# Kernel optimization log

Measured on AMD Instinct MI355X. Metric: run time of the kernel, lower is better.

The kernel has to match this reference:

```python
import jax, jax.numpy as jnp
import numpy as np

REG_MAX = 16
TOPK = 13
ALPHA = 1.0
BETA = 6.0
MATCH_W = 0.5
IOU_W = 7.5
DFL_W = 1.5
EPS = 1e-7
NEG_INF = -1e30


def _iou(b1, b2):
    # xyxy IoU, broadcastable [..., 4]
    x1 = jnp.maximum(b1[..., 0], b2[..., 0]); y1 = jnp.maximum(b1[..., 1], b2[..., 1])
    x2 = jnp.minimum(b1[..., 2], b2[..., 2]); y2 = jnp.minimum(b1[..., 3], b2[..., 3])
    inter = jnp.maximum(x2 - x1, 0.0) * jnp.maximum(y2 - y1, 0.0)
    a1 = (b1[..., 2] - b1[..., 0]) * (b1[..., 3] - b1[..., 1])
    a2 = (b2[..., 2] - b2[..., 0]) * (b2[..., 3] - b2[..., 1])
    return inter / (a1 + a2 - inter + EPS)


def _ciou(b1, b2):
    iou = _iou(b1, b2)
    w1 = b1[..., 2] - b1[..., 0]; h1 = b1[..., 3] - b1[..., 1]
    w2 = b2[..., 2] - b2[..., 0]; h2 = b2[..., 3] - b2[..., 1]
    cw = jnp.maximum(b1[..., 2], b2[..., 2]) - jnp.minimum(b1[..., 0], b2[..., 0])
    ch = jnp.maximum(b1[..., 3], b2[..., 3]) - jnp.minimum(b1[..., 1], b2[..., 1])
    c2 = cw * cw + ch * ch + EPS
    rho2 = ((b2[..., 0] + b2[..., 2] - b1[..., 0] - b1[..., 2]) ** 2
            + (b2[..., 1] + b2[..., 3] - b1[..., 1] - b1[..., 3]) ** 2) / 4.0
    v = (4.0 / jnp.pi ** 2) * (jnp.arctan(w2 / (h2 + EPS)) - jnp.arctan(w1 / (h1 + EPS))) ** 2
    a = jax.lax.stop_gradient(v / (v - iou + (1.0 + EPS)))
    return iou - (rho2 / c2 + v * a)


def _per_sample(ps, pb, bd, gtb, gtl, vcm, anchor, stride):
    # ps [N,C], pb [N,4], bd [N,4*R], gtb [M,4], gtl [M], vcm [C] bool
    N, C = ps.shape
    M = gtb.shape[0]
    lab = jnp.clip(gtl, 0, C - 1)
    gt_valid = (gtl >= 0) & (gtl < C) & vcm[lab]
    ax, ay = anchor[:, 0], anchor[:, 1]
    inside = ((ax[None, :] >= gtb[:, 0:1]) & (ax[None, :] <= gtb[:, 2:3])
              & (ay[None, :] >= gtb[:, 1:2]) & (ay[None, :] <= gtb[:, 3:4]))  # [M,N]
    iou_mn = _iou(pb[None, :, :], gtb[:, None, :])                             # [M,N]
    cls_mn = jax.nn.sigmoid(ps[:, lab]).T                                      # [M,N]
    align = jnp.where(inside & gt_valid[:, None], cls_mn ** ALPHA * iou_mn ** BETA, NEG_INF)
    top_vals, top_idx = jax.lax.top_k(align, TOPK)                             # [M,K]
    cand = jnp.full((M, N), NEG_INF, ps.dtype).at[jnp.arange(M)[:, None], top_idx].set(top_vals)
    best = cand.max(0)          # final metric per anchor
    mg = cand.argmax(0)         # winning GT (first max == earliest GT, matching loop order)
    fg = best > -1.0            # align >= 0 always; non-candidates stay at NEG_INF
    m_lab = jnp.clip(gtl[mg], 0, C - 1)
    ov = iou_mn[mg, jnp.arange(N)]
    fgf = fg.astype(ps.dtype)
    tgt_scores = jax.nn.one_hot(m_lab, C, dtype=ps.dtype) * (jnp.maximum(ov, 0.1) * fgf)[:, None]
    tb = jnp.where(fg[:, None], gtb[mg], pb)   # safe target boxes (masked out when not fg)

    # classification BCE over valid classes (mean)
    bce = jnp.maximum(ps, 0.0) - ps * tgt_scores + jnp.log1p(jnp.exp(-jnp.abs(ps)))
    vc = vcm.astype(ps.dtype)
    match = (bce * vc[None, :]).sum() / (N * jnp.maximum(vc.sum(), 1.0))

    cnt = fg.sum()
    ciou_v = _ciou(pb, tb)
    iou_loss = jnp.where(cnt > 0, ((1.0 - ciou_v) * fgf).sum() / jnp.maximum(cnt, 1), 0.0)
    miou_sum = (_iou(pb, tb) * fgf).sum()
    probs = jax.nn.sigmoid(ps)
    pos_sum = (probs[jnp.arange(N), m_lab] * fgf).sum()

    # DFL
    d = jnp.concatenate([anchor - tb[:, :2], tb[:, 2:] - anchor], -1) / stride  # [N,4]
    d = jnp.clip(d, 0.0, REG_MAX - 1 - 0.01)
    tl = d.astype(jnp.int32)
    tr = jnp.minimum(tl + 1, REG_MAX - 1)
    wl = tr.astype(ps.dtype) - d
    wr = 1.0 - wl
    logp = jax.nn.log_softmax(bd.reshape(N, 4, REG_MAX), -1)
    ll = -jnp.take_along_axis(logp, tl[..., None], -1)[..., 0]
    lr = -jnp.take_along_axis(logp, tr[..., None], -1)[..., 0]
    dfl = jnp.where(cnt > 0, ((ll * wl + lr * wr) * fgf[:, None]).sum() / jnp.maximum(cnt * 4, 1), 0.0)

    mx = jnp.where(vcm[None, :], probs, NEG_INF).max(-1)
    neg_sum = (mx * (1.0 - fgf)).sum()
    neg_cnt = N - cnt
    return match, iou_loss, dfl, cnt, neg_cnt, pos_sum, neg_sum, miou_sum


def setup_inputs() -> dict:
    key = jax.random.key(0)
    B, N, C, M, R = 16, 8400, 80, 64, REG_MAX
    ks = jax.random.split(key, 7)
    pts, sts = [], []
    for s in (8, 16, 32):
        n = 640 // s
        g = (np.arange(n) + 0.5) * s
        xv, yv = np.meshgrid(g, g)
        pts.append(np.stack([xv.ravel(), yv.ravel()], 1))
        sts.append(np.full((n * n, 1), s, np.float32))
    anchor_points = jnp.asarray(np.concatenate(pts).astype(np.float32))  # [8400,2]
    stride_tensor = jnp.asarray(np.concatenate(sts))                      # [8400,1]
    c = anchor_points[None] + jax.random.normal(ks[0], (B, N, 2)) * stride_tensor[None]
    wh = jax.random.uniform(ks[1], (B, N, 2), minval=8.0, maxval=128.0)
    pred_boxes = jnp.concatenate([jnp.clip(c - wh / 2, 0.0, 640.0),
                                  jnp.clip(c + wh / 2, 0.0, 640.0)], -1)
    gc = jax.random.uniform(ks[2], (B, M, 2), minval=64.0, maxval=576.0)
    gwh = jax.random.uniform(ks[3], (B, M, 2), minval=16.0, maxval=128.0)
    gt_boxes = jnp.concatenate([gc - gwh / 2, gc + gwh / 2], -1)
    gt_labels = jax.random.randint(ks[4], (B, M), 0, C)
    class_mask = jnp.ones((B, C), bool)
    pred_scores = jax.random.normal(ks[5], (B, N, C))
    box_distribution = jax.random.normal(ks[6], (B, N, 4 * R))
    return {"pred_scores": pred_scores, "pred_boxes": pred_boxes,
            "anchor_points": anchor_points, "stride_tensor": stride_tensor,
            "box_distribution": box_distribution, "gt_boxes": gt_boxes,
            "gt_labels": gt_labels, "class_mask": class_mask}


def reference(pred_scores, pred_boxes, anchor_points, stride_tensor,
              box_distribution, gt_boxes, gt_labels, class_mask):
    B = pred_scores.shape[0]
    f = lambda ps, pb, bd, gtb, gtl, vcm: _per_sample(ps, pb, bd, gtb, gtl, vcm,
                                                      anchor_points, stride_tensor)
    match, iou_l, dfl, cnt, ncnt, psum, nsum, misum = jax.vmap(f)(
        pred_scores, pred_boxes, box_distribution, gt_boxes, gt_labels, class_mask)
    tot_pos = cnt.sum()
    tot_neg = ncnt.sum()
    total_match = match.sum(); total_iou = iou_l.sum(); total_dfl = dfl.sum()
    loss = (MATCH_W * total_match + IOU_W * total_iou + DFL_W * total_dfl) / B
    mean_pos = psum.sum() / jnp.maximum(tot_pos, 1)
    mean_neg = nsum.sum() / jnp.maximum(tot_neg, 1)
    mean_miou = misum.sum() / jnp.maximum(tot_pos, 1)
    return (loss, total_match / B, total_iou / B, total_dfl / B,
            tot_pos.astype(jnp.float32), mean_pos, mean_neg, mean_miou)
```

## Files before the change

### kernel.cpp

```cpp
#include <hip/hip_runtime.h>
#include <stdint.h>

#define TOPK 13
#define NEG_INF_F (-1e30f)
#define EPSF 1e-7f
#define L2EF 1.4426950408889634f
#define LN2F 0.6931471805599453f
#define MAXCAND 2048
#define MAXB_LDS 64

__device__ __forceinline__ int mask_at(const uint8_t* __restrict__ raw, int i) {
    bool as_u8 = (raw[1] | raw[2] | raw[3]) != 0;
    return as_u8 ? (raw[i] != 0) : (((const int*)raw)[i] != 0);
}

__device__ __forceinline__ float iou_pair(float ax1, float ay1, float ax2, float ay2,
                                          float bx1, float by1, float bx2, float by2) {
    float x1 = fmaxf(ax1, bx1), y1 = fmaxf(ay1, by1);
    float x2 = fminf(ax2, bx2), y2 = fminf(ay2, by2);
    float inter = fmaxf(x2 - x1, 0.f) * fmaxf(y2 - y1, 0.f);
    float a1 = (ax2 - ax1) * (ay2 - ay1);
    float a2 = (bx2 - bx1) * (by2 - by1);
    return inter / (a1 + a2 - inter + EPSF);
}

__device__ __forceinline__ float sigmoid_fast(float s) {
    return 1.f / (1.f + exp2f(-s * L2EF));
}
__device__ __forceinline__ float softplus_bce(float s) {
    float t = exp2f(-fabsf(s) * L2EF);
    return fmaxf(s, 0.f) + log2f(1.f + t) * LN2F;
}

__device__ __forceinline__ void assign_wave(
    const float* __restrict__ ps, const float* __restrict__ pb,
    const float* __restrict__ gtb, const int* __restrict__ gtl,
    const uint8_t* __restrict__ mraw,
    unsigned long long* __restrict__ best, unsigned* __restrict__ list,
    int B, int N, int C, int M, int t, int lane) {
    int b = t % B;
    int m = t / B;

    int lbl = gtl[b * M + m];
    int lab = min(max(lbl, 0), C - 1);
    if (!((lbl >= 0) && (lbl < C) && (mask_at(mraw, b * C + lab) != 0))) return;

    float4 g = ((const float4*)gtb)[(size_t)b * M + m];

    const int   n0_[3]  = { 0, 6400, 8000 };
    const int   dim_[3] = { 80, 40, 20 };
    const float sv_[3]  = { 8.f, 16.f, 32.f };

    int ix0[3], iy0[3], ww[3], pre[4];
    pre[0] = 0;
#pragma unroll
    for (int l = 0; l < 3; ++l) {
        float s = sv_[l]; int d = dim_[l];
        int ax0 = max(0,     (int)ceilf (g.x / s - 0.5f));
        int ax1 = min(d - 1, (int)floorf(g.z / s - 0.5f));
        int ay0 = max(0,     (int)ceilf (g.y / s - 0.5f));
        int ay1 = min(d - 1, (int)floorf(g.w / s - 0.5f));
        int w = max(0, ax1 - ax0 + 1);
        int h = max(0, ay1 - ay0 + 1);
        ix0[l] = ax0; iy0[l] = ay0; ww[l] = w;
        pre[l + 1] = pre[l] + w * h;
    }
    int tot = pre[3];
    if (tot == 0) return;

    const float* psb = ps + (size_t)b * N * C + lab;
    const float4* pbb = (const float4*)pb + (size_t)b * N;

    float lv[TOPK];
    int   li[TOPK];
#pragma unroll
    for (int j = 0; j < TOPK; ++j) { lv[j] = NEG_INF_F; li[j] = -1; }

    for (int tt = lane; tt < tot; tt += 64) {
        int l = (tt >= pre[1]) + (tt >= pre[2]);
        int r = tt - pre[l];
        int w = ww[l];
        int iy = r / w, ix = r - iy * w;
        int gx = ix0[l] + ix, gy = iy0[l] + iy;
        int n = n0_[l] + gy * dim_[l] + gx;
        float4 p = pbb[n];
        float iou = iou_pair(p.x, p.y, p.z, p.w, g.x, g.y, g.z, g.w);
        float sc = psb[(size_t)n * C];
        float i3 = iou * iou * iou;
        float val = sigmoid_fast(sc) * i3 * i3;
        if (val > lv[TOPK - 1]) {
            bool placed = false;
#pragma unroll
            for (int j = TOPK - 1; j >= 1; --j) {
                if (!placed) {
                    if (val > lv[j - 1]) { lv[j] = lv[j - 1]; li[j] = li[j - 1]; }
                    else { lv[j] = val; li[j] = n; placed = true; }
                }
            }
            if (!placed) { lv[0] = val; li[0] = n; }
        }
    }

    unsigned key = 0xFFFFFFFFu - (unsigned)m;
    unsigned long long* bb = best + (size_t)b * N;
    unsigned* myslots = list + ((size_t)b * M + m) * TOPK;
    int rounds = min(tot, TOPK);
    for (int p = 0; p < rounds; ++p) {
        float bv = lv[0]; int bn = li[0];
        for (int off = 32; off > 0; off >>= 1) {
            float ov = __shfl_down(bv, off, 64);
            int   on = __shfl_down(bn, off, 64);
            if (ov > bv || (ov == bv && (unsigned)on < (unsigned)bn)) { bv = ov; bn = on; }
        }
        bv = __shfl(bv, 0, 64);
        bn = __shfl(bn, 0, 64);
        if (bn < 0) break;
        if (li[0] == bn) {
            unsigned long long pk =
                ((unsigned long long)__float_as_uint(lv[0]) << 32) | (unsigned long long)key;
            atomicMax(bb + bn, pk);
            myslots[p] = (unsigned)bn + 1u;
#pragma unroll
            for (int j = 0; j < TOPK - 1; ++j) { lv[j] = lv[j + 1]; li[j] = li[j + 1]; }
            lv[TOPK - 1] = NEG_INF_F; li[TOPK - 1] = -1;
        }
    }
}

__global__ __launch_bounds__(256, 1) void fused_a_k(
    const float* __restrict__ ps, const float* __restrict__ pb,
    const float* __restrict__ gtb, const int* __restrict__ gtl,
    const uint8_t* __restrict__ mraw,
    unsigned long long* __restrict__ best, unsigned* __restrict__ list,
    float* __restrict__ sigbuf, float* __restrict__ partials,
    int B, int N, int C, int M, int asgb, int nb) {
    if ((int)blockIdx.x < asgb) {
        int t = blockIdx.x * 4 + (threadIdx.x >> 6);
        if (t < B * M)
            assign_wave(ps, pb, gtb, gtl, mraw, best, list,
                        B, N, C, M, t, threadIdx.x & 63);
        return;
    }
    int bi = blockIdx.x - asgb;
    int b = bi / nb;
    int n = (bi % nb) * 256 + threadIdx.x;

    __shared__ int smask[256];
    __shared__ int s_notall;
    __shared__ float sredA[4], sredB[4];
    if (threadIdx.x == 0) s_notall = 0;
    __syncthreads();
    for (int c = threadIdx.x; c < C && c < 256; c += 256) {
        int v = mask_at(mraw, b * C + c);
        smask[c] = v;
        if (!v) s_notall = 1;
    }
    __syncthreads();
    bool allm = (s_notall == 0);

    float acc0 = 0.f, acc3 = 0.f;
    if (n < N) {
        const float* psr = ps + ((size_t)b * N + n) * C;
        float bce_sum = 0.f, smax = NEG_INF_F;

        if (C == 80 && allm) {
            const float4* p4 = (const float4*)psr;
            float4 s4[20];
#pragma unroll
            for (int i = 0; i < 20; ++i) s4[i] = p4[i];
#pragma unroll
            for (int i = 0; i < 20; ++i) {
                bce_sum += softplus_bce(s4[i].x) + softplus_bce(s4[i].y) +
                           softplus_bce(s4[i].z) + softplus_bce(s4[i].w);
                smax = fmaxf(smax, fmaxf(fmaxf(s4[i].x, s4[i].y), fmaxf(s4[i].z, s4[i].w)));
            }
        } else if (allm) {
            int c4 = C & ~3;
            for (int c = 0; c < c4; c += 4) {
                float4 s4 = *(const float4*)(psr + c);
                bce_sum += softplus_bce(s4.x) + softplus_bce(s4.y) +
                           softplus_bce(s4.z) + softplus_bce(s4.w);
                smax = fmaxf(smax, fmaxf(fmaxf(s4.x, s4.y), fmaxf(s4.z, s4.w)));
            }
            for (int c = c4; c < C; ++c) {
                float s = psr[c];
                bce_sum += softplus_bce(s);
                smax = fmaxf(smax, s);
            }
        } else {
            for (int c = 0; c < C; ++c) {
                float s = psr[c];
                if (smask[c]) { bce_sum += softplus_bce(s); smax = fmaxf(smax, s); }
            }
        }
        float sg = sigmoid_fast(smax);
        sigbuf[(size_t)b * N + n] = sg;
        acc0 = bce_sum;
        acc3 = sg;
    }

    int lane = threadIdx.x & 63, wid = threadIdx.x >> 6;
    float v0 = acc0, v3 = acc3;
    for (int off = 32; off > 0; off >>= 1) {
        v0 += __shfl_down(v0, off, 64);
        v3 += __shfl_down(v3, off, 64);
    }
    if (lane == 0) { sredA[wid] = v0; sredB[wid] = v3; }
    __syncthreads();
    if (threadIdx.x == 0) {
        atomicAdd(&partials[b * 8 + 0], sredA[0] + sredA[1] + sredA[2] + sredA[3]);
        atomicAdd(&partials[b * 8 + 3], sredB[0] + sredB[1] + sredB[2] + sredB[3]);
    }
}

__global__ __launch_bounds__(256, 1) void fused_b_k(
    const float* __restrict__ ps, const float* __restrict__ pb,
    const float* __restrict__ anch, const float* __restrict__ strd,
    const float* __restrict__ bd, const float* __restrict__ gtb,
    const int* __restrict__ gtl, const uint8_t* __restrict__ mraw,
    const unsigned long long* __restrict__ best, const float* __restrict__ sigbuf,
    const unsigned* __restrict__ list,
    float* __restrict__ partials, unsigned int* __restrict__ done_ctr,
    float* __restrict__ out, int B, int N, int C, int M) {
    __shared__ float sacc[MAXB_LDS * 8];
    __shared__ int s_last;
    bool use_lds = (B <= MAXB_LDS);
    if (use_lds)
        for (int i = threadIdx.x; i < B * 8; i += 256) sacc[i] = 0.f;
    __syncthreads();

    int idx = blockIdx.x * 256 + threadIdx.x;
    int cap = B * M * TOPK;
    bool active = false;
    int b = 0, n = 0, mg = 0;
    if (idx < cap) {
        unsigned e = list[idx];
        if (e != 0u) {
            n = (int)(e - 1u);
            b = idx / (M * TOPK);
            int m_claim = (idx / TOPK) % M;
            unsigned long long pk = best[(size_t)b * N + n];
            mg = (int)(0xFFFFFFFFu - (unsigned)(pk & 0xFFFFFFFFull));
            active = (mg == m_claim);
        }
    }

    if (active) {
        int lbl = gtl[b * M + mg];
        int m_lab = min(max(lbl, 0), C - 1);

        const float* bdr = bd + ((size_t)b * N + n) * 64;
        const float4* bq4 = (const float4*)bdr;
        float4 bq[16];
#pragma unroll
        for (int i = 0; i < 16; ++i) bq[i] = bq4[i];
        float4 p = ((const float4*)pb)[(size_t)b * N + n];
        float4 g = ((const float4*)gtb)[(size_t)b * M + mg];
        float2 an = ((const float2*)anch)[n];
        float stv = strd[n];
        float slab = ps[((size_t)b * N + n) * C + m_lab];
        float sg = sigbuf[(size_t)b * N + n];

        float ov = iou_pair(p.x, p.y, p.z, p.w, g.x, g.y, g.z, g.w);
        float acc0 = -fmaxf(ov, 0.1f) * slab;
        float acc2 = sigmoid_fast(slab);
        float acc4 = ov;
        float w1 = p.z - p.x, h1 = p.w - p.y;
        float w2 = g.z - g.x, h2 = g.w - g.y;
        float cw = fmaxf(p.z, g.z) - fminf(p.x, g.x);
        float ch = fmaxf(p.w, g.w) - fminf(p.y, g.y);
        float c2 = cw * cw + ch * ch + EPSF;
        float dx = g.x + g.z - p.x - p.z;
        float dy = g.y + g.w - p.y - p.w;
        float rho2 = (dx * dx + dy * dy) * 0.25f;
        const float PI = 3.14159265358979323846f;
        float dv = atanf(w2 / (h2 + EPSF)) - atanf(w1 / (h1 + EPSF));
        float v = (4.f / (PI * PI)) * dv * dv;
        float a = v / (v - ov + 1.f + EPSF);
        float acc5 = 1.f - (ov - (rho2 / c2 + v * a));
        float dall[4] = { (an.x - g.x) / stv, (an.y - g.y) / stv,
                          (g.z - an.x) / stv, (g.w - an.y) / stv };
        float dfl = 0.f;
#pragma unroll
        for (int k = 0; k < 4; ++k) {
            float4 q0 = bq[k * 4 + 0], q1 = bq[k * 4 + 1];
            float4 q2 = bq[k * 4 + 2], q3 = bq[k * 4 + 3];
            float mxv = fmaxf(fmaxf(fmaxf(q0.x, q0.y), fmaxf(q0.z, q0.w)),
                              fmaxf(fmaxf(q1.x, q1.y), fmaxf(q1.z, q1.w)));
            mxv = fmaxf(mxv, fmaxf(fmaxf(fmaxf(q2.x, q2.y), fmaxf(q2.z, q2.w)),
                                    fmaxf(fmaxf(q3.x, q3.y), fmaxf(q3.z, q3.w))));
            float se = exp2f((q0.x - mxv) * L2EF) + exp2f((q0.y - mxv) * L2EF) +
                       exp2f((q0.z - mxv) * L2EF) + exp2f((q0.w - mxv) * L2EF) +
                       exp2f((q1.x - mxv) * L2EF) + exp2f((q1.y - mxv) * L2EF) +
                       exp2f((q1.z - mxv) * L2EF) + exp2f((q1.w - mxv) * L2EF) +
                       exp2f((q2.x - mxv) * L2EF) + exp2f((q2.y - mxv) * L2EF) +
                       exp2f((q2.z - mxv) * L2EF) + exp2f((q2.w - mxv) * L2EF) +
                       exp2f((q3.x - mxv) * L2EF) + exp2f((q3.y - mxv) * L2EF) +
                       exp2f((q3.z - mxv) * L2EF) + exp2f((q3.w - mxv) * L2EF);
            float lse = mxv + log2f(se) * LN2F;
            float d = fminf(fmaxf(dall[k], 0.f), 14.99f);
            int tl = (int)d;
            int tr = min(tl + 1, 15);
            float wl = (float)tr - d;
            float xtl = bdr[k * 16 + tl];
            float xtr = bdr[k * 16 + tr];
            dfl += (lse - xtl) * wl + (lse - xtr) * (1.f - wl);
        }
        float accs[7] = { acc0, 1.f, acc2, -sg, acc4, acc5, dfl };
        if (use_lds) {
#pragma unroll
            for (int j = 0; j < 7; ++j) atomicAdd(&sacc[b * 8 + j], accs[j]);
        } else {
#pragma unroll
            for (int j = 0; j < 7; ++j) atomicAdd(&partials[b * 8 + j], accs[j]);
        }
    }
    __syncthreads();
    if (use_lds)
        for (int i = threadIdx.x; i < B * 8; i += 256)
            if (sacc[i] != 0.f) atomicAdd(&partials[i], sacc[i]);
    __syncthreads();

    if (threadIdx.x == 0) {
        __threadfence();
        unsigned r = atomicAdd(done_ctr, 1u);
        s_last = (r == gridDim.x - 1u) ? 1 : 0;
    }
    __syncthreads();
    if (!s_last) return;
    if (threadIdx.x >= 64) return;
    __threadfence();

    int fl = threadIdx.x;
    float tm = 0, ti = 0, td = 0, tp = 0, tneg = 0, pos = 0, neg = 0, miou = 0;
    for (int s = fl; s < B; s += 64) {
        float vcs = 0.f;
        for (int c = 0; c < C; ++c) vcs += mask_at(mraw, s * C + c) ? 1.f : 0.f;
        const float* pr = partials + s * 8;
        float p0 = __hip_atomic_load(&pr[0], __ATOMIC_RELAXED, __HIP_MEMORY_SCOPE_AGENT);
        float p1 = __hip_atomic_load(&pr[1], __ATOMIC_RELAXED, __HIP_MEMORY_SCOPE_AGENT);
        float p2 = __hip_atomic_load(&pr[2], __ATOMIC_RELAXED, __HIP_MEMORY_SCOPE_AGENT);
        float p3 = __hip_atomic_load(&pr[3], __ATOMIC_RELAXED, __HIP_MEMORY_SCOPE_AGENT);
        float p4 = __hip_atomic_load(&pr[4], __ATOMIC_RELAXED, __HIP_MEMORY_SCOPE_AGENT);
        float p5 = __hip_atomic_load(&pr[5], __ATOMIC_RELAXED, __HIP_MEMORY_SCOPE_AGENT);
        float p6 = __hip_atomic_load(&pr[6], __ATOMIC_RELAXED, __HIP_MEMORY_SCOPE_AGENT);
        float cnt = p1;
        tm += p0 / ((float)N * fmaxf(vcs, 1.f));
        ti += (cnt > 0.f) ? p5 / fmaxf(cnt, 1.f) : 0.f;
        td += (cnt > 0.f) ? p6 / fmaxf(cnt * 4.f, 1.f) : 0.f;
        tp += cnt; tneg += (float)N - cnt;
        pos += p2; neg += p3; miou += p4;
    }
    for (int off = 32; off > 0; off >>= 1) {
        tm += __shfl_down(tm, off, 64);   ti += __shfl_down(ti, off, 64);
        td += __shfl_down(td, off, 64);   tp += __shfl_down(tp, off, 64);
        tneg += __shfl_down(tneg, off, 64); pos += __shfl_down(pos, off, 64);
        neg += __shfl_down(neg, off, 64); miou += __shfl_down(miou, off, 64);
    }
    if (fl == 0) {
        float Bf = (float)B;
        out[0] = (0.5f * tm + 7.5f * ti + 1.5f * td) / Bf;
        out[1] = tm / Bf;
        out[2] = ti / Bf;
        out[3] = td / Bf;
        out[4] = tp;
        out[5] = pos / fmaxf(tp, 1.f);
        out[6] = neg / fmaxf(tneg, 1.f);
        out[7] = miou / fmaxf(tp, 1.f);
    }
}

__global__ __launch_bounds__(256) void assign_topk_k(
    const float* __restrict__ ps, const float* __restrict__ pb,
    const float* __restrict__ anch, const float* __restrict__ gtb,
    const int* __restrict__ gtl, const uint8_t* __restrict__ mraw,
    unsigned long long* __restrict__ best, int B, int N, int C, int M) {
    int b = blockIdx.x % B;
    int m = blockIdx.x / B;

    __shared__ float cval[MAXCAND];
    __shared__ int   cidx[MAXCAND];
    __shared__ int   scnt;
    if (threadIdx.x == 0) scnt = 0;

    int lbl = gtl[b * M + m];
    int lab = min(max(lbl, 0), C - 1);
    bool valid = (lbl >= 0) && (lbl < C) && (mask_at(mraw, b * C + lab) != 0);
    __syncthreads();

    if (valid) {
        float4 g = ((const float4*)gtb)[(size_t)b * M + m];
        const float* psb = ps + (size_t)b * N * C + lab;
        const float4* pbb = (const float4*)pb + (size_t)b * N;
        for (int n = threadIdx.x; n < N; n += 256) {
            float2 a = ((const float2*)anch)[n];
            if (a.x < g.x || a.x > g.z || a.y < g.y || a.y > g.w) continue;
            float4 p = pbb[n];
            float iou = iou_pair(p.x, p.y, p.z, p.w, g.x, g.y, g.z, g.w);
            float s = psb[(size_t)n * C];
            float i3 = iou * iou * iou;
            float val = sigmoid_fast(s) * i3 * i3;
            int slot = atomicAdd(&scnt, 1);
            if (slot < MAXCAND) { cval[slot] = val; cidx[slot] = n; }
        }
    }
    __syncthreads();
    if (!valid || threadIdx.x >= 64) return;

    int total = min(scnt, MAXCAND);
    if (total == 0) return;
    int lane = threadIdx.x;

    float lv[TOPK];
    int   li[TOPK];
#pragma unroll
    for (int j = 0; j < TOPK; ++j) { lv[j] = NEG_INF_F; li[j] = -1; }
    for (int i = lane; i < total; i += 64) {
        float v = cval[i]; int ix = cidx[i];
        if (v > lv[TOPK - 1]) {
            bool placed = false;
#pragma unroll
            for (int j = TOPK - 1; j >= 1; --j) {
                if (!placed) {
                    if (v > lv[j - 1]) { lv[j] = lv[j - 1]; li[j] = li[j - 1]; }
                    else { lv[j] = v; li[j] = ix; placed = true; }
                }
            }
            if (!placed) { lv[0] = v; li[0] = ix; }
        }
    }

    unsigned key = 0xFFFFFFFFu - (unsigned)m;
    unsigned long long* bb = best + (size_t)b * N;
    int rounds = min(total, TOPK);
    for (int p = 0; p < rounds; ++p) {
        float bv = lv[0]; int bn = li[0];
        for (int off = 32; off > 0; off >>= 1) {
            float ov = __shfl_down(bv, off, 64);
            int   on = __shfl_down(bn, off, 64);
            if (ov > bv || (ov == bv && (unsigned)on < (unsigned)bn)) { bv = ov; bn = on; }
        }
        bv = __shfl(bv, 0, 64);
        bn = __shfl(bn, 0, 64);
        if (bn < 0) break;
        if (li[0] == bn) {
            unsigned long long pk =
                ((unsigned long long)__float_as_uint(lv[0]) << 32) | (unsigned long long)key;
            atomicMax(bb + bn, pk);
#pragma unroll
            for (int j = 0; j < TOPK - 1; ++j) { lv[j] = lv[j + 1]; li[j] = li[j + 1]; }
            lv[TOPK - 1] = NEG_INF_F; li[TOPK - 1] = -1;
        }
    }
}

__global__ __launch_bounds__(256, 1) void per_anchor_k(
    const float* __restrict__ ps, const float* __restrict__ pb,
    const float* __restrict__ anch, const float* __restrict__ strd,
    const float* __restrict__ bd, const float* __restrict__ gtb,
    const int* __restrict__ gtl, const uint8_t* __restrict__ mraw,
    const unsigned long long* __restrict__ best,
    float* __restrict__ partials, int B, int N, int C, int M) {
    int b = blockIdx.y;
    int n = blockIdx.x * 256 + threadIdx.x;

    __shared__ int smask[256];
    __shared__ int s_notall;
    __shared__ float sred[4 * 8];
    if (threadIdx.x == 0) s_notall = 0;
    __syncthreads();
    for (int c = threadIdx.x; c < C && c < 256; c += 256) {
        int v = mask_at(mraw, b * C + c);
        smask[c] = v;
        if (!v) s_notall = 1;
    }
    __syncthreads();
    bool allm = (s_notall == 0);

    float acc0 = 0, acc1 = 0, acc2 = 0, acc3 = 0, acc4 = 0, acc5 = 0, acc6 = 0;

    if (n < N) {
        unsigned long long pk = best[(size_t)b * N + n];
        bool fg = (pk != 0ull);
        int mg = fg ? (int)(0xFFFFFFFFu - (unsigned)(pk & 0xFFFFFFFFull)) : 0;
        int lbl = gtl[b * M + mg];
        int m_lab = min(max(lbl, 0), C - 1);

        const float* psr = ps + ((size_t)b * N + n) * C;
        float bce_sum = 0.f, smax = NEG_INF_F;

        if (C == 80 && allm) {
            const float4* p4 = (const float4*)psr;
            float4 s4[20];
#pragma unroll
            for (int i = 0; i < 20; ++i) s4[i] = p4[i];
#pragma unroll
            for (int i = 0; i < 20; ++i) {
                bce_sum += softplus_bce(s4[i].x) + softplus_bce(s4[i].y) +
                           softplus_bce(s4[i].z) + softplus_bce(s4[i].w);
                smax = fmaxf(smax, fmaxf(fmaxf(s4[i].x, s4[i].y), fmaxf(s4[i].z, s4[i].w)));
            }
        } else if (allm) {
            int c4 = C & ~3;
            for (int c = 0; c < c4; c += 4) {
                float4 s4 = *(const float4*)(psr + c);
                bce_sum += softplus_bce(s4.x) + softplus_bce(s4.y) +
                           softplus_bce(s4.z) + softplus_bce(s4.w);
                smax = fmaxf(smax, fmaxf(fmaxf(s4.x, s4.y), fmaxf(s4.z, s4.w)));
            }
            for (int c = c4; c < C; ++c) {
                float s = psr[c];
                bce_sum += softplus_bce(s);
                smax = fmaxf(smax, s);
            }
        } else {
            for (int c = 0; c < C; ++c) {
                float s = psr[c];
                if (smask[c]) { bce_sum += softplus_bce(s); smax = fmaxf(smax, s); }
            }
        }

        acc1 = fg ? 1.f : 0.f;
        acc3 = fg ? 0.f : sigmoid_fast(smax);

        if (fg) {
            const float* bdr = bd + ((size_t)b * N + n) * 64;
            const float4* bq4 = (const float4*)bdr;
            float4 bq[16];
#pragma unroll
            for (int i = 0; i < 16; ++i) bq[i] = bq4[i];
            float4 p = ((const float4*)pb)[(size_t)b * N + n];
            float4 g = ((const float4*)gtb)[(size_t)b * M + mg];
            float2 an = ((const float2*)anch)[n];
            float stv = strd[n];
            float slab = psr[m_lab];

            float ov = iou_pair(p.x, p.y, p.z, p.w, g.x, g.y, g.z, g.w);
            bce_sum -= fmaxf(ov, 0.1f) * slab;
            acc2 = sigmoid_fast(slab);
            acc4 = ov;
            float w1 = p.z - p.x, h1 = p.w - p.y;
            float w2 = g.z - g.x, h2 = g.w - g.y;
            float cw = fmaxf(p.z, g.z) - fminf(p.x, g.x);
            float ch = fmaxf(p.w, g.w) - fminf(p.y, g.y);
            float c2 = cw * cw + ch * ch + EPSF;
            float dx = g.x + g.z - p.x - p.z;
            float dy = g.y + g.w - p.y - p.w;
            float rho2 = (dx * dx + dy * dy) * 0.25f;
            const float PI = 3.14159265358979323846f;
            float dv = atanf(w2 / (h2 + EPSF)) - atanf(w1 / (h1 + EPSF));
            float v = (4.f / (PI * PI)) * dv * dv;
            float a = v / (v - ov + 1.f + EPSF);
            acc5 = 1.f - (ov - (rho2 / c2 + v * a));
            float dall[4] = { (an.x - g.x) / stv, (an.y - g.y) / stv,
                              (g.z - an.x) / stv, (g.w - an.y) / stv };
            float dfl = 0.f;
#pragma unroll
            for (int k = 0; k < 4; ++k) {
                float4 q0 = bq[k * 4 + 0], q1 = bq[k * 4 + 1];
                float4 q2 = bq[k * 4 + 2], q3 = bq[k * 4 + 3];
                float mxv = fmaxf(fmaxf(fmaxf(q0.x, q0.y), fmaxf(q0.z, q0.w)),
                                  fmaxf(fmaxf(q1.x, q1.y), fmaxf(q1.z, q1.w)));
                mxv = fmaxf(mxv, fmaxf(fmaxf(fmaxf(q2.x, q2.y), fmaxf(q2.z, q2.w)),
                                        fmaxf(fmaxf(q3.x, q3.y), fmaxf(q3.z, q3.w))));
                float se = exp2f((q0.x - mxv) * L2EF) + exp2f((q0.y - mxv) * L2EF) +
                           exp2f((q0.z - mxv) * L2EF) + exp2f((q0.w - mxv) * L2EF) +
                           exp2f((q1.x - mxv) * L2EF) + exp2f((q1.y - mxv) * L2EF) +
                           exp2f((q1.z - mxv) * L2EF) + exp2f((q1.w - mxv) * L2EF) +
                           exp2f((q2.x - mxv) * L2EF) + exp2f((q2.y - mxv) * L2EF) +
                           exp2f((q2.z - mxv) * L2EF) + exp2f((q2.w - mxv) * L2EF) +
                           exp2f((q3.x - mxv) * L2EF) + exp2f((q3.y - mxv) * L2EF) +
                           exp2f((q3.z - mxv) * L2EF) + exp2f((q3.w - mxv) * L2EF);
                float lse = mxv + log2f(se) * LN2F;
                float d = fminf(fmaxf(dall[k], 0.f), 14.99f);
                int tl = (int)d;
                int tr = min(tl + 1, 15);
                float wl = (float)tr - d;
                float xtl = bdr[k * 16 + tl];
                float xtr = bdr[k * 16 + tr];
                dfl += (lse - xtl) * wl + (lse - xtr) * (1.f - wl);
            }
            acc6 = dfl;
        }
        acc0 = bce_sum;
    }

    int lane = threadIdx.x & 63, wid = threadIdx.x >> 6;
    float accs[7] = { acc0, acc1, acc2, acc3, acc4, acc5, acc6 };
#pragma unroll
    for (int j = 0; j < 7; ++j) {
        float v = accs[j];
        for (int off = 32; off > 0; off >>= 1) v += __shfl_down(v, off, 64);
        if (lane == 0) sred[wid * 8 + j] = v;
    }
    __syncthreads();
    if (threadIdx.x < 7) {
        float s = sred[0 * 8 + threadIdx.x] + sred[1 * 8 + threadIdx.x] +
                  sred[2 * 8 + threadIdx.x] + sred[3 * 8 + threadIdx.x];
        atomicAdd(&partials[b * 8 + threadIdx.x], s);
    }
}

__global__ void finalize_k(const float* __restrict__ partials, const uint8_t* __restrict__ mraw,
                           float* __restrict__ out, int B, int N, int C) {
    int lane = threadIdx.x;
    float tm = 0, ti = 0, td = 0, tp = 0, tneg = 0, pos = 0, neg = 0, miou = 0;
    if (lane < B) {
        float vcs = 0.f;
        for (int c = 0; c < C; ++c) vcs += mask_at(mraw, lane * C + c) ? 1.f : 0.f;
        const float* pr = partials + lane * 8;
        float cnt = pr[1];
        tm = pr[0] / ((float)N * fmaxf(vcs, 1.f));
        ti = (cnt > 0.f) ? pr[5] / fmaxf(cnt, 1.f) : 0.f;
        td = (cnt > 0.f) ? pr[6] / fmaxf(cnt * 4.f, 1.f) : 0.f;
        tp = cnt; tneg = (float)N - cnt;
        pos = pr[2]; neg = pr[3]; miou = pr[4];
    }
    for (int off = 32; off > 0; off >>= 1) {
        tm += __shfl_down(tm, off, 64);   ti += __shfl_down(ti, off, 64);
        td += __shfl_down(td, off, 64);   tp += __shfl_down(tp, off, 64);
        tneg += __shfl_down(tneg, off, 64); pos += __shfl_down(pos, off, 64);
        neg += __shfl_down(neg, off, 64); miou += __shfl_down(miou, off, 64);
    }
    if (lane == 0) {
        float Bf = (float)B;
        out[0] = (0.5f * tm + 7.5f * ti + 1.5f * td) / Bf;
        out[1] = tm / Bf;
        out[2] = ti / Bf;
        out[3] = td / Bf;
        out[4] = tp;
        out[5] = pos / fmaxf(tp, 1.f);
        out[6] = neg / fmaxf(tneg, 1.f);
        out[7] = miou / fmaxf(tp, 1.f);
    }
}

extern "C" void kernel_launch(void* const* d_in, const int* in_sizes, int n_in,
                              void* d_out, int out_size, void* d_ws, size_t ws_size,
                              hipStream_t stream) {
    const float* ps   = (const float*)d_in[0];
    const float* pb   = (const float*)d_in[1];
    const float* anch = (const float*)d_in[2];
    const float* strd = (const float*)d_in[3];
    const float* bd   = (const float*)d_in[4];
    const float* gtb  = (const float*)d_in[5];
    const int*   gtl  = (const int*)d_in[6];
    const uint8_t* cmsk = (const uint8_t*)d_in[7];

    int N = in_sizes[2] / 2;
    int B = in_sizes[1] / (4 * N);
    int C = in_sizes[0] / (B * N);
    int M = in_sizes[6] / B;

    size_t bestBytes = (size_t)B * N * sizeof(unsigned long long);
    size_t off1 = (bestBytes + 255) & ~(size_t)255;
    size_t partBytes = (size_t)B * 8 * sizeof(float);
    size_t off2 = (off1 + partBytes + 255) & ~(size_t)255;
    size_t off3 = off2 + 256;
    size_t listBytes = (size_t)B * M * TOPK * sizeof(unsigned);
    size_t zeroBytes = (off3 + listBytes + 255) & ~(size_t)255;
    unsigned long long* best = (unsigned long long*)d_ws;
    float* partials = (float*)((char*)d_ws + off1);
    unsigned int* done_ctr = (unsigned int*)((char*)d_ws + off2);
    unsigned int* list = (unsigned int*)((char*)d_ws + off3);
    float* sigbuf = (float*)((char*)d_ws + zeroBytes);

    hipMemsetAsync(d_ws, 0, zeroBytes, stream);

    int nb = (N + 255) / 256;
    if (N == 8400) {
        int asgb = (B * M + 3) / 4;
        fused_a_k<<<asgb + B * nb, 256, 0, stream>>>(ps, pb, gtb, gtl, cmsk,
                                                     best, list, sigbuf,
                                                     partials, B, N, C, M, asgb, nb);
        int cap = B * M * TOPK;
        int nblk = (cap + 255) / 256;
        fused_b_k<<<nblk, 256, 0, stream>>>(ps, pb, anch, strd, bd, gtb, gtl, cmsk,
                                            best, sigbuf, list,
                                            partials, done_ctr, (float*)d_out, B, N, C, M);
    } else {
        assign_topk_k<<<B * M, 256, 0, stream>>>(ps, pb, anch, gtb, gtl, cmsk, best, B, N, C, M);
        dim3 gB(nb, B);
        per_anchor_k<<<gB, 256, 0, stream>>>(ps, pb, anch, strd, bd, gtb, gtl, cmsk, best,
                                             partials, B, N, C, M);
        finalize_k<<<1, 64, 0, stream>>>(partials, cmsk, (float*)d_out, B, N, C);
    }
}
```

Measured before the change: 152.0 us.

## Merge assign/scan and foreground-loss kernels into one launch with grid-wide spin barrier

Fuses the two kernels on the N==8400 path into one mega-kernel. Each block bumps an atomic counter once its assignment or scan phase finishes. Scan blocks whose index falls within the candidate list then spin-wait on that counter before doing the foreground CIoU/DFL work. This removes one kernel launch and the gap between launches, but it relies on every block being co-resident to avoid deadlock. It also adds spin-wait latency and holds back some blocks.

```diff
diff --git a/kernel.cpp b/kernel.cpp
--- a/kernel.cpp
+++ b/kernel.cpp
@@ -127,27 +127,35 @@
     }
 }
 
-__global__ __launch_bounds__(256, 1) void fused_a_k(
+__global__ __launch_bounds__(256, 1) void mega_k(
     const float* __restrict__ ps, const float* __restrict__ pb,
-    const float* __restrict__ gtb, const int* __restrict__ gtl,
-    const uint8_t* __restrict__ mraw,
+    const float* __restrict__ anch, const float* __restrict__ strd,
+    const float* __restrict__ bd, const float* __restrict__ gtb,
+    const int* __restrict__ gtl, const uint8_t* __restrict__ mraw,
     unsigned long long* __restrict__ best, unsigned* __restrict__ list,
     float* __restrict__ sigbuf, float* __restrict__ partials,
-    int B, int N, int C, int M, int asgb, int nb) {
+    unsigned* __restrict__ a_done, unsigned* __restrict__ b_done,
+    float* __restrict__ out,
+    int B, int N, int C, int M, int asgb, int nb, int nscan, int cap) {
+    __shared__ int smask[256];
+    __shared__ int s_notall;
+    __shared__ float sredA[4], sredB[4];
+    __shared__ float sacc[MAXB_LDS * 8];
+    __shared__ int s_flag;
+
     if ((int)blockIdx.x < asgb) {
         int t = blockIdx.x * 4 + (threadIdx.x >> 6);
         if (t < B * M)
             assign_wave(ps, pb, gtb, gtl, mraw, best, list,
                         B, N, C, M, t, threadIdx.x & 63);
+        __syncthreads();
+        if (threadIdx.x == 0) { __threadfence(); atomicAdd(a_done, 1u); }
         return;
     }
     int bi = blockIdx.x - asgb;
     int b = bi / nb;
     int n = (bi % nb) * 256 + threadIdx.x;
 
-    __shared__ int smask[256];
-    __shared__ int s_notall;
-    __shared__ float sredA[4], sredB[4];
     if (threadIdx.x == 0) s_notall = 0;
     __syncthreads();
     for (int c = threadIdx.x; c < C && c < 256; c += 256) {
@@ -200,350 +208,79 @@
     }
 
     int lane = threadIdx.x & 63, wid = threadIdx.x >> 6;
-    float v0 = acc0, v3 = acc3;
-    for (int off = 32; off > 0; off >>= 1) {
-        v0 += __shfl_down(v0, off, 64);
-        v3 += __shfl_down(v3, off, 64);
-    }
-    if (lane == 0) { sredA[wid] = v0; sredB[wid] = v3; }
+    {
+        float v0 = acc0, v3 = acc3;
+        for (int off = 32; off > 0; off >>= 1) {
+            v0 += __shfl_down(v0, off, 64);
+            v3 += __shfl_down(v3, off, 64);
+        }
+        if (lane == 0) { sredA[wid] = v0; sredB[wid] = v3; }
+    }
     __syncthreads();
     if (threadIdx.x == 0) {
         atomicAdd(&partials[b * 8 + 0], sredA[0] + sredA[1] + sredA[2] + sredA[3]);
         atomicAdd(&partials[b * 8 + 3], sredB[0] + sredB[1] + sredB[2] + sredB[3]);
-    }
-}
-
-__global__ __launch_bounds__(256, 1) void fused_b_k(
-    const float* __restrict__ ps, const float* __restrict__ pb,
-    const float* __restrict__ anch, const float* __restrict__ strd,
-    const float* __restrict__ bd, const float* __restrict__ gtb,
-    const int* __restrict__ gtl, const uint8_t* __restrict__ mraw,
-    const unsigned long long* __restrict__ best, const float* __restrict__ sigbuf,
-    const unsigned* __restrict__ list,
-    float* __restrict__ partials, unsigned int* __restrict__ done_ctr,
-    float* __restrict__ out, int B, int N, int C, int M) {
-    __shared__ float sacc[MAXB_LDS * 8];
-    __shared__ int s_last;
+        __threadfence();
+        atomicAdd(a_done, 1u);
+    }
+
+    int base = bi * 256;
     bool use_lds = (B <= MAXB_LDS);
-    if (use_lds)
-        for (int i = threadIdx.x; i < B * 8; i += 256) sacc[i] = 0.f;
-    __syncthreads();
-
-    int idx = blockIdx.x * 256 + threadIdx.x;
-    int cap = B * M * TOPK;
-    bool active = false;
-    int b = 0, n = 0, mg = 0;
-    if (idx < cap) {
-        unsigned e = list[idx];
-        if (e != 0u) {
-            n = (int)(e - 1u);
-            b = idx / (M * TOPK);
-            int m_claim = (idx / TOPK) % M;
-            unsigned long long pk = best[(size_t)b * N + n];
-            mg = (int)(0xFFFFFFFFu - (unsigned)(pk & 0xFFFFFFFFull));
-            active = (mg == m_claim);
-        }
-    }
-
-    if (active) {
-        int lbl = gtl[b * M + mg];
-        int m_lab = min(max(lbl, 0), C - 1);
-
-        const float* bdr = bd + ((size_t)b * N + n) * 64;
-        const float4* bq4 = (const float4*)bdr;
-        float4 bq[16];
-#pragma unroll
-        for (int i = 0; i < 16; ++i) bq[i] = bq4[i];
-        float4 p = ((const float4*)pb)[(size_t)b * N + n];
-        float4 g = ((const float4*)gtb)[(size_t)b * M + mg];
-        float2 an = ((const float2*)anch)[n];
-        float stv = strd[n];
-        float slab = ps[((size_t)b * N + n) * C + m_lab];
-        float sg = sigbuf[(size_t)b * N + n];
-
-        float ov = iou_pair(p.x, p.y, p.z, p.w, g.x, g.y, g.z, g.w);
-        float acc0 = -fmaxf(ov, 0.1f) * slab;
-        float acc2 = sigmoid_fast(slab);
-        float acc4 = ov;
-        float w1 = p.z - p.x, h1 = p.w - p.y;
-        float w2 = g.z - g.x, h2 = g.w - g.y;
-        float cw = fmaxf(p.z, g.z) - fminf(p.x, g.x);
-        float ch = fmaxf(p.w, g.w) - fminf(p.y, g.y);
-        float c2 = cw * cw + ch * ch + EPSF;
-        float dx = g.x + g.z - p.x - p.z;
-        float dy = g.y + g.w - p.y - p.w;
-        float rho2 = (dx * dx + dy * dy) * 0.25f;
-        const float PI = 3.14159265358979323846f;
-        float dv = atanf(w2 / (h2 + EPSF)) - atanf(w1 / (h1 + EPSF));
-        float v = (4.f / (PI * PI)) * dv * dv;
-        float a = v / (v - ov + 1.f + EPSF);
-        float acc5 = 1.f - (ov - (rho2 / c2 + v * a));
-        float dall[4] = { (an.x - g.x) / stv, (an.y - g.y) / stv,
-                          (g.z - an.x) / stv, (g.w - an.y) / stv };
-        float dfl = 0.f;
-#pragma unroll
-        for (int k = 0; k < 4; ++k) {
-            float4 q0 = bq[k * 4 + 0], q1 = bq[k * 4 + 1];
-            float4 q2 = bq[k * 4 + 2], q3 = bq[k * 4 + 3];
-            float mxv = fmaxf(fmaxf(fmaxf(q0.x, q0.y), fmaxf(q0.z, q0.w)),
-                              fmaxf(fmaxf(q1.x, q1.y), fmaxf(q1.z, q1.w)));
-            mxv = fmaxf(mxv, fmaxf(fmaxf(fmaxf(q2.x, q2.y), fmaxf(q2.z, q2.w)),
-                                    fmaxf(fmaxf(q3.x, q3.y), fmaxf(q3.z, q3.w))));
-            float se = exp2f((q0.x - mxv) * L2EF) + exp2f((q0.y - mxv) * L2EF) +
-                       exp2f((q0.z - mxv) * L2EF) + exp2f((q0.w - mxv) * L2EF) +
-                       exp2f((q1.x - mxv) * L2EF) + exp2f((q1.y - mxv) * L2EF) +
-                       exp2f((q1.z - mxv) * L2EF) + exp2f((q1.w - mxv) * L2EF) +
-                       exp2f((q2.x - mxv) * L2EF) + exp2f((q2.y - mxv) * L2EF) +
-                       exp2f((q2.z - mxv) * L2EF) + exp2f((q2.w - mxv) * L2EF) +
-                       exp2f((q3.x - mxv) * L2EF) + exp2f((q3.y - mxv) * L2EF) +
-                       exp2f((q3.z - mxv) * L2EF) + exp2f((q3.w - mxv) * L2EF);
-            float lse = mxv + log2f(se) * LN2F;
-            float d = fminf(fmaxf(dall[k], 0.f), 14.99f);
-            int tl = (int)d;
-            int tr = min(tl + 1, 15);
-            float wl = (float)tr - d;
-            float xtl = bdr[k * 16 + tl];
-            float xtr = bdr[k * 16 + tr];
-            dfl += (lse - xtl) * wl + (lse - xtr) * (1.f - wl);
-        }
-        float accs[7] = { acc0, 1.f, acc2, -sg, acc4, acc5, dfl };
-        if (use_lds) {
-#pragma unroll
-            for (int j = 0; j < 7; ++j) atomicAdd(&sacc[b * 8 + j], accs[j]);
-        } else {
-#pragma unroll
-            for (int j = 0; j < 7; ++j) atomicAdd(&partials[b * 8 + j], accs[j]);
-        }
-    }
-    __syncthreads();
-    if (use_lds)
-        for (int i = threadIdx.x; i < B * 8; i += 256)
-            if (sacc[i] != 0.f) atomicAdd(&partials[i], sacc[i]);
-    __syncthreads();
-
-    if (threadIdx.x == 0) {
+    if (base < cap) {
+        if (threadIdx.x == 0) {
+            int a_target = asgb + nscan;
+            while ((int)__hip_atomic_load(a_done, __ATOMIC_ACQUIRE,
+                                          __HIP_MEMORY_SCOPE_AGENT) < a_target)
+                __builtin_amdgcn_s_sleep(8);
+            s_flag = 1;
+        }
+        __syncthreads();
         __threadfence();
-        unsigned r = atomicAdd(done_ctr, 1u);
-        s_last = (r == gridDim.x - 1u) ? 1 : 0;
-    }
-    __syncthreads();
-    if (!s_last) return;
-    if (threadIdx.x >= 64) return;
-    __threadfence();
-
-    int fl = threadIdx.x;
-    float tm = 0, ti = 0, td = 0, tp = 0, tneg = 0, pos = 0, neg = 0, miou = 0;
-    for (int s = fl; s < B; s += 64) {
-        float vcs = 0.f;
-        for (int c = 0; c < C; ++c) vcs += mask_at(mraw, s * C + c) ? 1.f : 0.f;
-        const float* pr = partials + s * 8;
-        float p0 = __hip_atomic_load(&pr[0], __ATOMIC_RELAXED, __HIP_MEMORY_SCOPE_AGENT);
-        float p1 = __hip_atomic_load(&pr[1], __ATOMIC_RELAXED, __HIP_MEMORY_SCOPE_AGENT);
-        float p2 = __hip_atomic_load(&pr[2], __ATOMIC_RELAXED, __HIP_MEMORY_SCOPE_AGENT);
-        float p3 = __hip_atomic_load(&pr[3], __ATOMIC_RELAXED, __HIP_MEMORY_SCOPE_AGENT);
-        float p4 = __hip_atomic_load(&pr[4], __ATOMIC_RELAXED, __HIP_MEMORY_SCOPE_AGENT);
-        float p5 = __hip_atomic_load(&pr[5], __ATOMIC_RELAXED, __HIP_MEMORY_SCOPE_AGENT);
-        float p6 = __hip_atomic_load(&pr[6], __ATOMIC_RELAXED, __HIP_MEMORY_SCOPE_AGENT);
-        float cnt = p1;
-        tm += p0 / ((float)N * fmaxf(vcs, 1.f));
-        ti += (cnt > 0.f) ? p5 / fmaxf(cnt, 1.f) : 0.f;
-        td += (cnt > 0.f) ? p6 / fmaxf(cnt * 4.f, 1.f) : 0.f;
-        tp += cnt; tneg += (float)N - cnt;
-        pos += p2; neg += p3; miou += p4;
-    }
-    for (int off = 32; off > 0; off >>= 1) {
-        tm += __shfl_down(tm, off, 64);   ti += __shfl_down(ti, off, 64);
-        td += __shfl_down(td, off, 64);   tp += __shfl_down(tp, off, 64);
-        tneg += __shfl_down(tneg, off, 64); pos += __shfl_down(pos, off, 64);
-        neg += __shfl_down(neg, off, 64); miou += __shfl_down(miou, off, 64);
-    }
-    if (fl == 0) {
-        float Bf = (float)B;
-        out[0] = (0.5f * tm + 7.5f * ti + 1.5f * td) / Bf;
-        out[1] = tm / Bf;
-        out[2] = ti / Bf;
-        out[3] = td / Bf;
-        out[4] = tp;
-        out[5] = pos / fmaxf(tp, 1.f);
-        out[6] = neg / fmaxf(tneg, 1.f);
-        out[7] = miou / fmaxf(tp, 1.f);
-    }
-}
-
-__global__ __launch_bounds__(256) void assign_topk_k(
-    const float* __restrict__ ps, const float* __restrict__ pb,
-    const float* __restrict__ anch, const float* __restrict__ gtb,
-    const int* __restrict__ gtl, const uint8_t* __restrict__ mraw,
-    unsigned long long* __restrict__ best, int B, int N, int C, int M) {
-    int b = blockIdx.x % B;
-    int m = blockIdx.x / B;
-
-    __shared__ float cval[MAXCAND];
-    __shared__ int   cidx[MAXCAND];
-    __shared__ int   scnt;
-    if (threadIdx.x == 0) scnt = 0;
-
-    int lbl = gtl[b * M + m];
-    int lab = min(max(lbl, 0), C - 1);
-    bool valid = (lbl >= 0) && (lbl < C) && (mask_at(mraw, b * C + lab) != 0);
-    __syncthreads();
-
-    if (valid) {
-        float4 g = ((const float4*)gtb)[(size_t)b * M + m];
-        const float* psb = ps + (size_t)b * N * C + lab;
-        const float4* pbb = (const float4*)pb + (size_t)b * N;
-        for (int n = threadIdx.x; n < N; n += 256) {
-            float2 a = ((const float2*)anch)[n];
-            if (a.x < g.x || a.x > g.z || a.y < g.y || a.y > g.w) continue;
-            float4 p = pbb[n];
-            float iou = iou_pair(p.x, p.y, p.z, p.w, g.x, g.y, g.z, g.w);
-            float s = psb[(size_t)n * C];
-            float i3 = iou * iou * iou;
-            float val = sigmoid_fast(s) * i3 * i3;
-            int slot = atomicAdd(&scnt, 1);
-            if (slot < MAXCAND) { cval[slot] = val; cidx[slot] = n; }
-        }
-    }
-    __syncthreads();
-    if (!valid || threadIdx.x >= 64) return;
-
-    int total = min(scnt, MAXCAND);
-    if (total == 0) return;
-    int lane = threadIdx.x;
-
-    float lv[TOPK];
-    int   li[TOPK];
-#pragma unroll
-    for (int j = 0; j < TOPK; ++j) { lv[j] = NEG_INF_F; li[j] = -1; }
-    for (int i = lane; i < total; i += 64) {
-        float v = cval[i]; int ix = cidx[i];
-        if (v > lv[TOPK - 1]) {
-            bool placed = false;
-#pragma unroll
-            for (int j = TOPK - 1; j >= 1; --j) {
-                if (!placed) {
-                    if (v > lv[j - 1]) { lv[j] = lv[j - 1]; li[j] = li[j - 1]; }
-                    else { lv[j] = v; li[j] = ix; placed = true; }
-                }
-            }
-            if (!placed) { lv[0] = v; li[0] = ix; }
-        }
-    }
-
-    unsigned key = 0xFFFFFFFFu - (unsigned)m;
-    unsigned long long* bb = best + (size_t)b * N;
-    int rounds = min(total, TOPK);
-    for (int p = 0; p < rounds; ++p) {
-        float bv = lv[0]; int bn = li[0];
-        for (int off = 32; off > 0; off >>= 1) {
-            float ov = __shfl_down(bv, off, 64);
-            int   on = __shfl_down(bn, off, 64);
-            if (ov > bv || (ov == bv && (unsigned)on < (unsigned)bn)) { bv = ov; bn = on; }
-        }
-        bv = __shfl(bv, 0, 64);
-        bn = __shfl(bn, 0, 64);
-        if (bn < 0) break;
-        if (li[0] == bn) {
-            unsigned long long pk =
-                ((unsigned long long)__float_as_uint(lv[0]) << 32) | (unsigned long long)key;
-            atomicMax(bb + bn, pk);
-#pragma unroll
-            for (int j = 0; j < TOPK - 1; ++j) { lv[j] = lv[j + 1]; li[j] = li[j + 1]; }
-            lv[TOPK - 1] = NEG_INF_F; li[TOPK - 1] = -1;
-        }
-    }
-}
-
-__global__ __launch_bounds__(256, 1) void per_anchor_k(
-    const float* __restrict__ ps, const float* __restrict__ pb,
-    const float* __restrict__ anch, const float* __restrict__ strd,
-    const float* __restrict__ bd, const float* __restrict__ gtb,
-    const int* __restrict__ gtl, const uint8_t* __restrict__ mraw,
-    const unsigned long long* __restrict__ best,
-    float* __restrict__ partials, int B, int N, int C, int M) {
-    int b = blockIdx.y;
-    int n = blockIdx.x * 256 + threadIdx.x;
-
-    __shared__ int smask[256];
-    __shared__ int s_notall;
-    __shared__ float sred[4 * 8];
-    if (threadIdx.x == 0) s_notall = 0;
-    __syncthreads();
-    for (int c = threadIdx.x; c < C && c < 256; c += 256) {
-        int v = mask_at(mraw, b * C + c);
-        smask[c] = v;
-        if (!v) s_notall = 1;
-    }
-    __syncthreads();
-    bool allm = (s_notall == 0);
-
-    float acc0 = 0, acc1 = 0, acc2 = 0, acc3 = 0, acc4 = 0, acc5 = 0, acc6 = 0;
-
-    if (n < N) {
-        unsigned long long pk = best[(size_t)b * N + n];
-        bool fg = (pk != 0ull);
-        int mg = fg ? (int)(0xFFFFFFFFu - (unsigned)(pk & 0xFFFFFFFFull)) : 0;
-        int lbl = gtl[b * M + mg];
-        int m_lab = min(max(lbl, 0), C - 1);
-
-        const float* psr = ps + ((size_t)b * N + n) * C;
-        float bce_sum = 0.f, smax = NEG_INF_F;
-
-        if (C == 80 && allm) {
-            const float4* p4 = (const float4*)psr;
-            float4 s4[20];
-#pragma unroll
-            for (int i = 0; i < 20; ++i) s4[i] = p4[i];
-#pragma unroll
-            for (int i = 0; i < 20; ++i) {
-                bce_sum += softplus_bce(s4[i].x) + softplus_bce(s4[i].y) +
-                           softplus_bce(s4[i].z) + softplus_bce(s4[i].w);
-                smax = fmaxf(smax, fmaxf(fmaxf(s4[i].x, s4[i].y), fmaxf(s4[i].z, s4[i].w)));
-            }
-        } else if (allm) {
-            int c4 = C & ~3;
-            for (int c = 0; c < c4; c += 4) {
-                float4 s4 = *(const float4*)(psr + c);
-                bce_sum += softplus_bce(s4.x) + softplus_bce(s4.y) +
-                           softplus_bce(s4.z) + softplus_bce(s4.w);
-                smax = fmaxf(smax, fmaxf(fmaxf(s4.x, s4.y), fmaxf(s4.z, s4.w)));
-            }
-            for (int c = c4; c < C; ++c) {
-                float s = psr[c];
-                bce_sum += softplus_bce(s);
-                smax = fmaxf(smax, s);
-            }
-        } else {
-            for (int c = 0; c < C; ++c) {
-                float s = psr[c];
-                if (smask[c]) { bce_sum += softplus_bce(s); smax = fmaxf(smax, s); }
-            }
-        }
-
-        acc1 = fg ? 1.f : 0.f;
-        acc3 = fg ? 0.f : sigmoid_fast(smax);
-
-        if (fg) {
-            const float* bdr = bd + ((size_t)b * N + n) * 64;
+
+        if (use_lds)
+            for (int i = threadIdx.x; i < B * 8; i += 256) sacc[i] = 0.f;
+        __syncthreads();
+
+        int idx = base + threadIdx.x;
+        bool active = false;
+        int fb = 0, fn = 0, mg = 0;
+        if (idx < cap) {
+            unsigned e = list[idx];
+            if (e != 0u) {
+                fn = (int)(e - 1u);
+                fb = idx / (M * TOPK);
+                int m_claim = (idx / TOPK) % M;
+                unsigned long long pk = best[(size_t)fb * N + fn];
+                mg = (int)(0xFFFFFFFFu - (unsigned)(pk & 0xFFFFFFFFull));
+                active = (mg == m_claim);
+            }
+        }
+
+        if (active) {
+            int lbl = gtl[fb * M + mg];
+            int m_lab = min(max(lbl, 0), C - 1);
+
+            const float* bdr = bd + ((size_t)fb * N + fn) * 64;
             const float4* bq4 = (const float4*)bdr;
             float4 bq[16];
 #pragma unroll
             for (int i = 0; i < 16; ++i) bq[i] = bq4[i];
-            float4 p = ((const float4*)pb)[(size_t)b * N + n];
-            float4 g = ((const float4*)gtb)[(size_t)b * M + mg];
-            float2 an = ((const float2*)anch)[n];
-            float stv = strd[n];
-            float slab = psr[m_lab];
+            float4 p = ((const float4*)pb)[(size_t)fb * N + fn];
+            float4 g = ((const float4*)gtb)[(size_t)fb * M + mg];
+            float2 an = ((const float2*)anch)[fn];
+            float stv = strd[fn];
+            float slab = ps[((size_t)fb * N + fn) * C + m_lab];
+            float sg = sigbuf[(size_t)fb * N + fn];
 
             float ov = iou_pair(p.x, p.y, p.z, p.w, g.x, g.y, g.z, g.w);
-            bce_sum -= fmaxf(ov, 0.1f) * slab;
-            acc2 = sigmoid_fast(slab);
-            acc4 = ov;
+            float c0 = -fmaxf(ov, 0.1f) * slab;
+            float c2 = sigmoid_fast(slab);
+            float c4 = ov;
             float w1 = p.z - p.x, h1 = p.w - p.y;
             float w2 = g.z - g.x, h2 = g.w - g.y;
             float cw = fmaxf(p.z, g.z) - fminf(p.x, g.x);
             float ch = fmaxf(p.w, g.w) - fminf(p.y, g.y);
-            float c2 = cw * cw + ch * ch + EPSF;
+            float cc2 = cw * cw + ch * ch + EPSF;
             float dx = g.x + g.z - p.x - p.z;
             float dy = g.y + g.w - p.y - p.w;
             float rho2 = (dx * dx + dy * dy) * 0.25f;
@@ -551,7 +288,7 @@
             float dv = atanf(w2 / (h2 + EPSF)) - atanf(w1 / (h1 + EPSF));
             float v = (4.f / (PI * PI)) * dv * dv;
             float a = v / (v - ov + 1.f + EPSF);
-            acc5 = 1.f - (ov - (rho2 / c2 + v * a));
+            float c5 = 1.f - (ov - (rho2 / cc2 + v * a));
             float dall[4] = { (an.x - g.x) / stv, (an.y - g.y) / stv,
                               (g.z - an.x) / stv, (g.w - an.y) / stv };
             float dfl = 0.f;
@@ -580,6 +317,281 @@
                 float xtr = bdr[k * 16 + tr];
                 dfl += (lse - xtl) * wl + (lse - xtr) * (1.f - wl);
             }
+            float accs[7] = { c0, 1.f, c2, -sg, c4, c5, dfl };
+            if (use_lds) {
+#pragma unroll
+                for (int j = 0; j < 7; ++j) atomicAdd(&sacc[fb * 8 + j], accs[j]);
+            } else {
+#pragma unroll
+                for (int j = 0; j < 7; ++j) atomicAdd(&partials[fb * 8 + j], accs[j]);
+            }
+        }
+        __syncthreads();
+        if (use_lds)
+            for (int i = threadIdx.x; i < B * 8; i += 256)
+                if (sacc[i] != 0.f) atomicAdd(&partials[i], sacc[i]);
+        __syncthreads();
+    }
+
+    if (threadIdx.x == 0) {
+        __threadfence();
+        unsigned r = atomicAdd(b_done, 1u);
+        s_flag = (r == (unsigned)nscan - 1u) ? 1 : 0;
+    }
+    __syncthreads();
+    if (!s_flag) return;
+    if (threadIdx.x >= 64) return;
+    __threadfence();
+
+    int fl = threadIdx.x;
+    float tm = 0, ti = 0, td = 0, tp = 0, tneg = 0, pos = 0, neg = 0, miou = 0;
+    for (int s = fl; s < B; s += 64) {
+        float vcs = 0.f;
+        for (int c = 0; c < C; ++c) vcs += mask_at(mraw, s * C + c) ? 1.f : 0.f;
+        const float* pr = partials + s * 8;
+        float p0 = __hip_atomic_load(&pr[0], __ATOMIC_RELAXED, __HIP_MEMORY_SCOPE_AGENT);
+        float p1 = __hip_atomic_load(&pr[1], __ATOMIC_RELAXED, __HIP_MEMORY_SCOPE_AGENT);
+        float p2 = __hip_atomic_load(&pr[2], __ATOMIC_RELAXED, __HIP_MEMORY_SCOPE_AGENT);
+        float p3 = __hip_atomic_load(&pr[3], __ATOMIC_RELAXED, __HIP_MEMORY_SCOPE_AGENT);
+        float p4 = __hip_atomic_load(&pr[4], __ATOMIC_RELAXED, __HIP_MEMORY_SCOPE_AGENT);
+        float p5 = __hip_atomic_load(&pr[5], __ATOMIC_RELAXED, __HIP_MEMORY_SCOPE_AGENT);
+        float p6 = __hip_atomic_load(&pr[6], __ATOMIC_RELAXED, __HIP_MEMORY_SCOPE_AGENT);
+        float cnt = p1;
+        tm += p0 / ((float)N * fmaxf(vcs, 1.f));
+        ti += (cnt > 0.f) ? p5 / fmaxf(cnt, 1.f) : 0.f;
+        td += (cnt > 0.f) ? p6 / fmaxf(cnt * 4.f, 1.f) : 0.f;
+        tp += cnt; tneg += (float)N - cnt;
+        pos += p2; neg += p3; miou += p4;
+    }
+    for (int off = 32; off > 0; off >>= 1) {
+        tm += __shfl_down(tm, off, 64);   ti += __shfl_down(ti, off, 64);
+        td += __shfl_down(td, off, 64);   tp += __shfl_down(tp, off, 64);
+        tneg += __shfl_down(tneg, off, 64); pos += __shfl_down(pos, off, 64);
+        neg += __shfl_down(neg, off, 64); miou += __shfl_down(miou, off, 64);
+    }
+    if (fl == 0) {
+        float Bf = (float)B;
+        out[0] = (0.5f * tm + 7.5f * ti + 1.5f * td) / Bf;
+        out[1] = tm / Bf;
+        out[2] = ti / Bf;
+        out[3] = td / Bf;
+        out[4] = tp;
+        out[5] = pos / fmaxf(tp, 1.f);
+        out[6] = neg / fmaxf(tneg, 1.f);
+        out[7] = miou / fmaxf(tp, 1.f);
+    }
+}
+
+__global__ __launch_bounds__(256) void assign_topk_k(
+    const float* __restrict__ ps, const float* __restrict__ pb,
+    const float* __restrict__ anch, const float* __restrict__ gtb,
+    const int* __restrict__ gtl, const uint8_t* __restrict__ mraw,
+    unsigned long long* __restrict__ best, int B, int N, int C, int M) {
+    int b = blockIdx.x % B;
+    int m = blockIdx.x / B;
+
+    __shared__ float cval[MAXCAND];
+    __shared__ int   cidx[MAXCAND];
+    __shared__ int   scnt;
+    if (threadIdx.x == 0) scnt = 0;
+
+    int lbl = gtl[b * M + m];
+    int lab = min(max(lbl, 0), C - 1);
+    bool valid = (lbl >= 0) && (lbl < C) && (mask_at(mraw, b * C + lab) != 0);
+    __syncthreads();
+
+    if (valid) {
+        float4 g = ((const float4*)gtb)[(size_t)b * M + m];
+        const float* psb = ps + (size_t)b * N * C + lab;
+        const float4* pbb = (const float4*)pb + (size_t)b * N;
+        for (int n = threadIdx.x; n < N; n += 256) {
+            float2 a = ((const float2*)anch)[n];
+            if (a.x < g.x || a.x > g.z || a.y < g.y || a.y > g.w) continue;
+            float4 p = pbb[n];
+            float iou = iou_pair(p.x, p.y, p.z, p.w, g.x, g.y, g.z, g.w);
+            float s = psb[(size_t)n * C];
+            float i3 = iou * iou * iou;
+            float val = sigmoid_fast(s) * i3 * i3;
+            int slot = atomicAdd(&scnt, 1);
+            if (slot < MAXCAND) { cval[slot] = val; cidx[slot] = n; }
+        }
+    }
+    __syncthreads();
+    if (!valid || threadIdx.x >= 64) return;
+
+    int total = min(scnt, MAXCAND);
+    if (total == 0) return;
+    int lane = threadIdx.x;
+
+    float lv[TOPK];
+    int   li[TOPK];
+#pragma unroll
+    for (int j = 0; j < TOPK; ++j) { lv[j] = NEG_INF_F; li[j] = -1; }
+    for (int i = lane; i < total; i += 64) {
+        float v = cval[i]; int ix = cidx[i];
+        if (v > lv[TOPK - 1]) {
+            bool placed = false;
+#pragma unroll
+            for (int j = TOPK - 1; j >= 1; --j) {
+                if (!placed) {
+                    if (v > lv[j - 1]) { lv[j] = lv[j - 1]; li[j] = li[j - 1]; }
+                    else { lv[j] = v; li[j] = ix; placed = true; }
+                }
+            }
+            if (!placed) { lv[0] = v; li[0] = ix; }
+        }
+    }
+
+    unsigned key = 0xFFFFFFFFu - (unsigned)m;
+    unsigned long long* bb = best + (size_t)b * N;
+    int rounds = min(total, TOPK);
+    for (int p = 0; p < rounds; ++p) {
+        float bv = lv[0]; int bn = li[0];
+        for (int off = 32; off > 0; off >>= 1) {
+            float ov = __shfl_down(bv, off, 64);
+            int   on = __shfl_down(bn, off, 64);
+            if (ov > bv || (ov == bv && (unsigned)on < (unsigned)bn)) { bv = ov; bn = on; }
+        }
+        bv = __shfl(bv, 0, 64);
+        bn = __shfl(bn, 0, 64);
+        if (bn < 0) break;
+        if (li[0] == bn) {
+            unsigned long long pk =
+                ((unsigned long long)__float_as_uint(lv[0]) << 32) | (unsigned long long)key;
+            atomicMax(bb + bn, pk);
+#pragma unroll
+            for (int j = 0; j < TOPK - 1; ++j) { lv[j] = lv[j + 1]; li[j] = li[j + 1]; }
+            lv[TOPK - 1] = NEG_INF_F; li[TOPK - 1] = -1;
+        }
+    }
+}
+
+__global__ __launch_bounds__(256, 1) void per_anchor_k(
+    const float* __restrict__ ps, const float* __restrict__ pb,
+    const float* __restrict__ anch, const float* __restrict__ strd,
+    const float* __restrict__ bd, const float* __restrict__ gtb,
+    const int* __restrict__ gtl, const uint8_t* __restrict__ mraw,
+    const unsigned long long* __restrict__ best,
+    float* __restrict__ partials, int B, int N, int C, int M) {
+    int b = blockIdx.y;
+    int n = blockIdx.x * 256 + threadIdx.x;
+
+    __shared__ int smask[256];
+    __shared__ int s_notall;
+    __shared__ float sred[4 * 8];
+    if (threadIdx.x == 0) s_notall = 0;
+    __syncthreads();
+    for (int c = threadIdx.x; c < C && c < 256; c += 256) {
+        int v = mask_at(mraw, b * C + c);
+        smask[c] = v;
+        if (!v) s_notall = 1;
+    }
+    __syncthreads();
+    bool allm = (s_notall == 0);
+
+    float acc0 = 0, acc1 = 0, acc2 = 0, acc3 = 0, acc4 = 0, acc5 = 0, acc6 = 0;
+
+    if (n < N) {
+        unsigned long long pk = best[(size_t)b * N + n];
+        bool fg = (pk != 0ull);
+        int mg = fg ? (int)(0xFFFFFFFFu - (unsigned)(pk & 0xFFFFFFFFull)) : 0;
+        int lbl = gtl[b * M + mg];
+        int m_lab = min(max(lbl, 0), C - 1);
+
+        const float* psr = ps + ((size_t)b * N + n) * C;
+        float bce_sum = 0.f, smax = NEG_INF_F;
+
+        if (C == 80 && allm) {
+            const float4* p4 = (const float4*)psr;
+            float4 s4[20];
+#pragma unroll
+            for (int i = 0; i < 20; ++i) s4[i] = p4[i];
+#pragma unroll
+            for (int i = 0; i < 20; ++i) {
+                bce_sum += softplus_bce(s4[i].x) + softplus_bce(s4[i].y) +
+                           softplus_bce(s4[i].z) + softplus_bce(s4[i].w);
+                smax = fmaxf(smax, fmaxf(fmaxf(s4[i].x, s4[i].y), fmaxf(s4[i].z, s4[i].w)));
+            }
+        } else if (allm) {
+            int c4 = C & ~3;
+            for (int c = 0; c < c4; c += 4) {
+                float4 s4 = *(const float4*)(psr + c);
+                bce_sum += softplus_bce(s4.x) + softplus_bce(s4.y) +
+                           softplus_bce(s4.z) + softplus_bce(s4.w);
+                smax = fmaxf(smax, fmaxf(fmaxf(s4.x, s4.y), fmaxf(s4.z, s4.w)));
+            }
+            for (int c = c4; c < C; ++c) {
+                float s = psr[c];
+                bce_sum += softplus_bce(s);
+                smax = fmaxf(smax, s);
+            }
+        } else {
+            for (int c = 0; c < C; ++c) {
+                float s = psr[c];
+                if (smask[c]) { bce_sum += softplus_bce(s); smax = fmaxf(smax, s); }
+            }
+        }
+
+        acc1 = fg ? 1.f : 0.f;
+        acc3 = fg ? 0.f : sigmoid_fast(smax);
+
+        if (fg) {
+            const float* bdr = bd + ((size_t)b * N + n) * 64;
+            const float4* bq4 = (const float4*)bdr;
+            float4 bq[16];
+#pragma unroll
+            for (int i = 0; i < 16; ++i) bq[i] = bq4[i];
+            float4 p = ((const float4*)pb)[(size_t)b * N + n];
+            float4 g = ((const float4*)gtb)[(size_t)b * M + mg];
+            float2 an = ((const float2*)anch)[n];
+            float stv = strd[n];
+            float slab = psr[m_lab];
+
+            float ov = iou_pair(p.x, p.y, p.z, p.w, g.x, g.y, g.z, g.w);
+            bce_sum -= fmaxf(ov, 0.1f) * slab;
+            acc2 = sigmoid_fast(slab);
+            acc4 = ov;
+            float w1 = p.z - p.x, h1 = p.w - p.y;
+            float w2 = g.z - g.x, h2 = g.w - g.y;
+            float cw = fmaxf(p.z, g.z) - fminf(p.x, g.x);
+            float ch = fmaxf(p.w, g.w) - fminf(p.y, g.y);
+            float c2 = cw * cw + ch * ch + EPSF;
+            float dx = g.x + g.z - p.x - p.z;
+            float dy = g.y + g.w - p.y - p.w;
+            float rho2 = (dx * dx + dy * dy) * 0.25f;
+            const float PI = 3.14159265358979323846f;
+            float dv = atanf(w2 / (h2 + EPSF)) - atanf(w1 / (h1 + EPSF));
+            float v = (4.f / (PI * PI)) * dv * dv;
+            float a = v / (v - ov + 1.f + EPSF);
+            acc5 = 1.f - (ov - (rho2 / c2 + v * a));
+            float dall[4] = { (an.x - g.x) / stv, (an.y - g.y) / stv,
+                              (g.z - an.x) / stv, (g.w - an.y) / stv };
+            float dfl = 0.f;
+#pragma unroll
+            for (int k = 0; k < 4; ++k) {
+                float4 q0 = bq[k * 4 + 0], q1 = bq[k * 4 + 1];
+                float4 q2 = bq[k * 4 + 2], q3 = bq[k * 4 + 3];
+                float mxv = fmaxf(fmaxf(fmaxf(q0.x, q0.y), fmaxf(q0.z, q0.w)),
+                                  fmaxf(fmaxf(q1.x, q1.y), fmaxf(q1.z, q1.w)));
+                mxv = fmaxf(mxv, fmaxf(fmaxf(fmaxf(q2.x, q2.y), fmaxf(q2.z, q2.w)),
+                                        fmaxf(fmaxf(q3.x, q3.y), fmaxf(q3.z, q3.w))));
+                float se = exp2f((q0.x - mxv) * L2EF) + exp2f((q0.y - mxv) * L2EF) +
+                           exp2f((q0.z - mxv) * L2EF) + exp2f((q0.w - mxv) * L2EF) +
+                           exp2f((q1.x - mxv) * L2EF) + exp2f((q1.y - mxv) * L2EF) +
+                           exp2f((q1.z - mxv) * L2EF) + exp2f((q1.w - mxv) * L2EF) +
+                           exp2f((q2.x - mxv) * L2EF) + exp2f((q2.y - mxv) * L2EF) +
+                           exp2f((q2.z - mxv) * L2EF) + exp2f((q2.w - mxv) * L2EF) +
+                           exp2f((q3.x - mxv) * L2EF) + exp2f((q3.y - mxv) * L2EF) +
+                           exp2f((q3.z - mxv) * L2EF) + exp2f((q3.w - mxv) * L2EF);
+                float lse = mxv + log2f(se) * LN2F;
+                float d = fminf(fmaxf(dall[k], 0.f), 14.99f);
+                int tl = (int)d;
+                int tr = min(tl + 1, 15);
+                float wl = (float)tr - d;
+                float xtl = bdr[k * 16 + tl];
+                float xtr = bdr[k * 16 + tr];
+                dfl += (lse - xtl) * wl + (lse - xtr) * (1.f - wl);
+            }
             acc6 = dfl;
         }
         acc0 = bce_sum;
@@ -661,7 +673,8 @@
     size_t zeroBytes = (off3 + listBytes + 255) & ~(size_t)255;
     unsigned long long* best = (unsigned long long*)d_ws;
     float* partials = (float*)((char*)d_ws + off1);
-    unsigned int* done_ctr = (unsigned int*)((char*)d_ws + off2);
+    unsigned int* a_done = (unsigned int*)((char*)d_ws + off2);
+    unsigned int* b_done = a_done + 1;
     unsigned int* list = (unsigned int*)((char*)d_ws + off3);
     float* sigbuf = (float*)((char*)d_ws + zeroBytes);
 
@@ -670,14 +683,12 @@
     int nb = (N + 255) / 256;
     if (N == 8400) {
         int asgb = (B * M + 3) / 4;
-        fused_a_k<<<asgb + B * nb, 256, 0, stream>>>(ps, pb, gtb, gtl, cmsk,
-                                                     best, list, sigbuf,
-                                                     partials, B, N, C, M, asgb, nb);
+        int nscan = B * nb;
         int cap = B * M * TOPK;
-        int nblk = (cap + 255) / 256;
-        fused_b_k<<<nblk, 256, 0, stream>>>(ps, pb, anch, strd, bd, gtb, gtl, cmsk,
-                                            best, sigbuf, list,
-                                            partials, done_ctr, (float*)d_out, B, N, C, M);
+        mega_k<<<asgb + nscan, 256, 0, stream>>>(ps, pb, anch, strd, bd, gtb, gtl, cmsk,
+                                                 best, list, sigbuf, partials,
+                                                 a_done, b_done, (float*)d_out,
+                                                 B, N, C, M, asgb, nb, nscan, cap);
     } else {
         assign_topk_k<<<B * M, 256, 0, stream>>>(ps, pb, anch, gtb, gtl, cmsk, best, B, N, C, M);
         dim3 gB(nb, B);
```

Measured after the change: 208.5 us. +37.2%, slower.
